# Kernel tuning notes

Hardware: AMD Instinct MI355X
Metric: run time of the kernel (lower is better)

## Reference

```python
import jax, jax.numpy as jnp
import numpy as np

B, D, F, P = 65536, 256, 512, 256


def setup_inputs() -> dict:
    key = jax.random.key(0)
    k_x, k_f, k_p, k_a, k_b, k_t = jax.random.split(key, 6)
    x = jax.random.normal(k_x, (B, D), dtype=jnp.float32)
    # reset_parameters: uniform(-0.27, 1)
    features = jax.random.uniform(k_f, (F, D), dtype=jnp.float32, minval=-0.27, maxval=1.0)
    prototypes = jax.random.uniform(k_p, (P, D), dtype=jnp.float32, minval=-0.27, maxval=1.0)
    # alpha/beta/theta init to zeros in the module; use small random values so the
    # output is non-trivial for kernel correctness checking.
    alpha = jax.random.normal(k_a, (1,), dtype=jnp.float32) * 0.1
    beta = jax.random.normal(k_b, (1,), dtype=jnp.float32) * 0.1
    theta = jax.random.normal(k_t, (1,), dtype=jnp.float32) * 0.1
    return {"x": x, "features": features, "prototypes": prototypes,
            "alpha": alpha, "beta": beta, "theta": theta}


def reference(x, features, prototypes, alpha, beta, theta):
    # Shared projections
    x_features = x @ features.T                 # [B, F]
    p_features = prototypes @ features.T        # [P, F]
    x_present = jax.nn.relu(x_features)         # [B, F]
    p_present = jax.nn.relu(p_features)         # [P, F]
    x_weighted = x_features * x_present         # [B, F]
    p_weighted = p_features * p_present         # [P, F]

    # Tversky terms
    common = x_weighted @ p_weighted.T                          # [B, P]
    x_weighted_sum = jnp.sum(x_weighted, axis=1, keepdims=True)  # [B, 1]
    x_p_interaction = x_weighted @ p_present.T                  # [B, P]
    x_distinctive = x_weighted_sum - x_p_interaction            # [B, P]
    p_weighted_sum = jnp.sum(p_weighted, axis=1)[None, :]        # [1, P]
    x_p_weighted_interaction = x_present @ p_weighted.T         # [B, P]
    p_distinctive = p_weighted_sum - x_p_weighted_interaction   # [B, P]

    return theta * common - alpha * x_distinctive - beta * p_distinctive
```

## Files before the change

### kernel.cpp

```cpp
#include <hip/hip_runtime.h>
#include <cstdint>
#include <cstddef>

#define Bsz 65536
#define Dsz 256
#define Fsz 512
#define Psz 256

typedef __attribute__((ext_vector_type(8))) short short8;
typedef __attribute__((ext_vector_type(4))) short short4v;
typedef __attribute__((ext_vector_type(4))) float float4v;
typedef __attribute__((ext_vector_type(16))) float float16v;
typedef __attribute__((ext_vector_type(4))) unsigned uint4v;

__device__ inline short f2bf(float f) {
    unsigned u = __builtin_bit_cast(unsigned, f);
    u = (u + 0x7FFFu + ((u >> 16) & 1u)) >> 16;
    return (short)u;
}
__device__ inline float bf2f(short s) {
    unsigned u = ((unsigned)(unsigned short)s) << 16;
    return __builtin_bit_cast(float, u);
}
__device__ inline unsigned cvt_pk_bf16(float lo, float hi) {
    unsigned r;
    asm("v_cvt_pk_bf16_f32 %0, %1, %2" : "=v"(r) : "v"(lo), "v"(hi));
    return r;
}
__device__ inline void gl_lds16(const short* g, short* lds) {
    __builtin_amdgcn_global_load_lds((const __attribute__((address_space(1))) unsigned*)g,
                                     (__attribute__((address_space(3))) unsigned*)lds,
                                     16, 0, 0);
}


#define SBPITCH 136

__global__ __launch_bounds__(256, 2) void k_pre(
    const float* __restrict__ prototypes, const float* __restrict__ features,
    const float* __restrict__ alpha_p, const float* __restrict__ beta_p,
    const float* __restrict__ theta_p,
    short* __restrict__ featbB, short* __restrict__ pab, float* __restrict__ pws_part)
{
    __shared__ char lds[65536 + 17408];
    short* FB = (short*)lds;
    short* As = (short*)(lds + 65536);
    short* Sb = (short*)(lds + 65536);

    const int t = threadIdx.x;
    const int w = t >> 6, lane = t & 63, l15 = lane & 15, l4 = lane >> 4;
    const int rowg = blockIdx.x >> 2, nc = blockIdx.x & 3;
    const float alpha = *alpha_p, beta = *beta_p, theta = *theta_p;

    #pragma unroll
    for (int it = 0; it < 16; ++it) {
        int u = it * 256 + t;
        int ftl = u >> 10, dtl = (u >> 6) & 15, ln = u & 63;
        const float* src = features + (size_t)(nc * 128 + ftl * 32 + (ln & 31)) * Dsz
                         + dtl * 16 + (ln >> 5) * 8;
        float4v v0 = *(const float4v*)src;
        float4v v1 = *(const float4v*)(src + 4);
        uint4v uv;
        uv.x = cvt_pk_bf16(v0.x, v0.y);
        uv.y = cvt_pk_bf16(v0.z, v0.w);
        uv.z = cvt_pk_bf16(v1.x, v1.y);
        uv.w = cvt_pk_bf16(v1.z, v1.w);
        short8 sv = __builtin_bit_cast(short8, uv);
        *(short8*)&FB[u * 8] = sv;
        if (rowg == 0) {
            int go = (((nc * 4 + ftl) * 16 + dtl) * 64 + ln) * 8;
            *(short8*)&featbB[go] = sv;
        }
    }

    float4v acc[2][4];
    #pragma unroll
    for (int a = 0; a < 2; ++a)
        #pragma unroll
        for (int b = 0; b < 4; ++b) acc[a][b] = (float4v){0.f, 0.f, 0.f, 0.f};

    const float* pbase = prototypes + (size_t)rowg * 64 * Dsz;

    for (int kc = 0; kc < 4; ++kc) {
        __syncthreads();
        #pragma unroll
        for (int j = 0; j < 4; ++j) {
            int idx = j * 1024 + t * 4;
            int r = idx >> 6, c = idx & 63;
            float4v v = *(const float4v*)(pbase + (size_t)r * Dsz + kc * 64 + c);
            int unit = r * 8 + ((c >> 3) ^ (r & 7));
            short4v s4; s4.x = f2bf(v.x); s4.y = f2bf(v.y); s4.z = f2bf(v.z); s4.w = f2bf(v.w);
            *(short4v*)((char*)As + unit * 16 + (c & 7) * 2) = s4;
        }
        __syncthreads();
        #pragma unroll
        for (int kk = 0; kk < 2; ++kk) {
            short8 af[2], bfr[4];
            const int k8 = kk * 4 + l4;
            #pragma unroll
            for (int tm = 0; tm < 2; ++tm) {
                int m = (w & 1) * 32 + tm * 16 + l15;
                af[tm] = *(const short8*)&As[(m * 8 + (k8 ^ (m & 7))) * 8];
            }
            #pragma unroll
            for (int tn = 0; tn < 4; ++tn) {
                int fl = ((w >> 1) * 4 + tn) * 16 + l15;
                int dtl = kc * 4 + kk * 2 + (l4 >> 1);
                int lnp = (fl & 31) + 32 * (l4 & 1);
                bfr[tn] = *(const short8*)&FB[(((fl >> 5) * 16 + dtl) * 64 + lnp) * 8];
            }
            #pragma unroll
            for (int tm = 0; tm < 2; ++tm)
                #pragma unroll
                for (int tn = 0; tn < 4; ++tn)
                    acc[tm][tn] = __builtin_amdgcn_mfma_f32_16x16x32_bf16(af[tm], bfr[tn], acc[tm][tn], 0, 0, 0);
        }
    }
    __syncthreads();
    #pragma unroll
    for (int tm = 0; tm < 2; ++tm)
        #pragma unroll
        for (int tn = 0; tn < 4; ++tn)
            #pragma unroll
            for (int r = 0; r < 4; ++r) {
                int row = (w & 1) * 32 + tm * 16 + l4 * 4 + r;
                int col = (w >> 1) * 64 + tn * 16 + l15;
                Sb[row * SBPITCH + col] = f2bf(acc[tm][tn][r]);
            }
    __syncthreads();
    #pragma unroll
    for (int rep = 0; rep < 4; ++rep) {
        int u = rep * 256 + t;
        int row = u >> 4, i = u & 15;
        short8 sv = *(const short8*)&Sb[row * SBPITCH + i * 8];
        uint4v u0, u1;
        float sum = 0.f;
        #pragma unroll
        for (int e = 0; e < 8; ++e) {
            float pf = bf2f(sv[e]);
            float pp = fmaxf(pf, 0.f);
            float pw = pf * pp;
            float a0 = theta * pw + alpha * (pp - 1.f);
            float b0 = beta * pw;
            sum += pw;
            unsigned pk = cvt_pk_bf16(a0, b0);
            if (e < 4) u0[e] = pk; else u1[e - 4] = pk;
        }
        int p = rowg * 64 + row;
        int c = 4 * nc + (i >> 2), s2 = i & 3, pt = p >> 5;
        int base = ((c * 4 + s2) * 8 + pt) * 512;
        *(short8*)&pab[base + (p & 31) * 8] = __builtin_bit_cast(short8, u0);
        *(short8*)&pab[base + ((p & 31) + 32) * 8] = __builtin_bit_cast(short8, u1);
        #pragma unroll
        for (int mk = 1; mk < 16; mk <<= 1) sum += __shfl_xor(sum, mk, 64);
        if (l15 == 0) pws_part[nc * 256 + p] = -beta * sum;
    }
}

__global__ __launch_bounds__(256, 2) void k_main(
    const float* __restrict__ x, const short* __restrict__ featbB,
    const short* __restrict__ pab, const float* __restrict__ pws_part,
    float* __restrict__ out)
{
    __shared__ short XL[16384];
    __shared__ short FBL[16384];

    const int t = threadIdx.x;
    const int w = t >> 6, lane = t & 63, l31 = lane & 31, h = lane >> 5;
    const size_t row0 = (size_t)blockIdx.x * 64;

    #pragma unroll
    for (int it = 0; it < 8; ++it) {
        int idx = it * 256 + t;
        int mt_i = idx >> 10, dt_i = (idx >> 6) & 15, ln = idx & 63;
        const float* src = x + (row0 + mt_i * 32 + (ln & 31)) * Dsz + dt_i * 16 + (ln >> 5) * 8;
        float4v v0 = *(const float4v*)src;
        float4v v1 = *(const float4v*)(src + 4);
        uint4v uv;
        uv.x = cvt_pk_bf16(v0.x, v0.y);
        uv.y = cvt_pk_bf16(v0.z, v0.w);
        uv.z = cvt_pk_bf16(v1.x, v1.y);
        uv.w = cvt_pk_bf16(v1.z, v1.w);
        *(short8*)&XL[idx * 8] = __builtin_bit_cast(short8, uv);
    }

    #pragma unroll
    for (int i = 0; i < 4; ++i) {
        int dt = w * 4 + i;
        gl_lds16(featbB + dt * 512 + lane * 8, &FBL[dt * 512]);
    }
    __syncthreads();

    const int mt = w & 1, pth = w >> 1;
    int xbase = mt * 8192 + lane * 8;
    const int lane8 = lane * 8;
    const int pboff = (pth * 4) * 512 + lane8;

    short8 xlo[8];
    #pragma unroll
    for (int dt = 0; dt < 8; ++dt)
        xlo[dt] = *(const short8*)&XL[xbase + dt * 512];

    float16v acc[4];
    #pragma unroll
    for (int a = 0; a < 4; ++a)
        #pragma unroll
        for (int e = 0; e < 16; ++e) acc[a][e] = 0.f;

    short8 PB[16];
    #pragma unroll
    for (int ptl = 0; ptl < 4; ++ptl)
        #pragma unroll
        for (int s = 0; s < 4; ++s)
            PB[ptl * 4 + s] = *(const short8*)(pab + pboff + s * 4096 + ptl * 512);

    #pragma unroll 1
    for (int c = 0; c < 16; ++c) {
        const int buf = (c & 1) * 8192;
        const int cn = (c + 1) & 15;

        if (c) __syncthreads();
        asm volatile("" : "+v"(xbase));

        {
            const short* gsrc = featbB + (size_t)cn * 8192 + lane8;
            short* ldst = &FBL[buf ^ 8192];
            #pragma unroll
            for (int i = 0; i < 4; ++i) {
                int dt = w * 4 + i;
                gl_lds16(gsrc + dt * 512, ldst + dt * 512);
            }
        }

        float16v C1;
        #pragma unroll
        for (int e = 0; e < 16; ++e) C1[e] = 0.f;
        #pragma unroll
        for (int g = 0; g < 4; ++g) {
            short8 fbf[4];
            #pragma unroll
            for (int i = 0; i < 4; ++i)
                fbf[i] = *(const short8*)&FBL[buf + (g * 4 + i) * 512 + lane8];
            __builtin_amdgcn_s_setprio(1);
            #pragma unroll
            for (int i = 0; i < 4; ++i) {
                const int dt = g * 4 + i;
                short8 xf = (dt < 8) ? xlo[dt] : *(const short8*)&XL[xbase + dt * 512];
                C1 = __builtin_amdgcn_mfma_f32_32x32x16_bf16(fbf[i], xf, C1, 0, 0, 0);
            }
            __builtin_amdgcn_s_setprio(0);
        }

        #pragma unroll
        for (int s = 0; s < 4; ++s) {
            uint4v uf;
            #pragma unroll
            for (int q = 0; q < 4; ++q) {
                float xf = C1[4 * s + q];
                float xp = fmaxf(xf, 0.f);
                uf[q] = cvt_pk_bf16(xf * xp, xp);
            }
            short8 A2f = __builtin_bit_cast(short8, uf);
            __builtin_amdgcn_s_setprio(1);
            #pragma unroll
            for (int ptl = 0; ptl < 4; ++ptl)
                acc[ptl] = __builtin_amdgcn_mfma_f32_32x32x16_bf16(A2f, PB[ptl * 4 + s], acc[ptl], 0, 0, 0);
            __builtin_amdgcn_s_setprio(0);
        }

        {
            const short* pbn = pab + (size_t)cn * 16384 + pboff;
            #pragma unroll
            for (int ptl = 0; ptl < 4; ++ptl)
                #pragma unroll
                for (int s = 0; s < 4; ++s)
                    PB[ptl * 4 + s] = *(const short8*)(pbn + s * 4096 + ptl * 512);
        }
    }

    #pragma unroll
    for (int ptl = 0; ptl < 4; ++ptl) {
        int pcol = (pth * 4 + ptl) * 32 + l31;
        float pn = pws_part[pcol] + pws_part[256 + pcol] + pws_part[512 + pcol] + pws_part[768 + pcol];
        #pragma unroll
        for (int r = 0; r < 16; ++r) {
            size_t m = row0 + mt * 32 + (r & 3) + 8 * (r >> 2) + 4 * h;
            out[m * Psz + pcol] = acc[ptl][r] + pn;
        }
    }
}

extern "C" void kernel_launch(void* const* d_in, const int* in_sizes, int n_in,
                              void* d_out, int out_size, void* d_ws, size_t ws_size,
                              hipStream_t stream) {
    const float* x          = (const float*)d_in[0];
    const float* features   = (const float*)d_in[1];
    const float* prototypes = (const float*)d_in[2];
    const float* alpha      = (const float*)d_in[3];
    const float* beta       = (const float*)d_in[4];
    const float* theta      = (const float*)d_in[5];
    float* out = (float*)d_out;

    char* ws = (char*)d_ws;
    short* featbB   = (short*)(ws);
    short* pab      = (short*)(ws + 262144);
    float* pws_part = (float*)(ws + 786432);

    hipLaunchKernelGGL(k_pre,  dim3(16),   dim3(256), 0, stream,
                       prototypes, features, alpha, beta, theta, featbB, pab, pws_part);
    hipLaunchKernelGGL(k_main, dim3(1024), dim3(256), 0, stream,
                       x, featbB, pab, pws_part, out);
}
```

Measured before the change: 192.7 us.

## Enlarge block to 128 rows, keep x in registers, stage prototypes in LDS

Each block now covers 128 rows with 512 threads (8 waves, 4 row tiles by 2 prototype halves). Each wave loads its x rows directly into registers as bf16 fragments instead of going through LDS. The precomputed prototype operand is double-buffered in LDS alongside the features chunk, replacing per-wave global register loads. The first GEMM is split across two accumulators to break the MFMA dependency chain. The goal is to halve feature/prototype traffic per row and cut global-load latency, at the cost of more LDS and register pressure, which may limit occupancy.

```diff
diff --git a/kernel.cpp b/kernel.cpp
--- a/kernel.cpp
+++ b/kernel.cpp
@@ -157,130 +157,126 @@
     }
 }
 
-__global__ __launch_bounds__(256, 2) void k_main(
+__global__ __launch_bounds__(512, 2) void k_main(
     const float* __restrict__ x, const short* __restrict__ featbB,
     const short* __restrict__ pab, const float* __restrict__ pws_part,
     float* __restrict__ out)
 {
-    __shared__ short XL[16384];
-    __shared__ short FBL[16384];
+    __shared__ short FBL[2][8192];
+    __shared__ short PBL[2][16384];
 
     const int t = threadIdx.x;
     const int w = t >> 6, lane = t & 63, l31 = lane & 31, h = lane >> 5;
-    const size_t row0 = (size_t)blockIdx.x * 64;
-
-    #pragma unroll
-    for (int it = 0; it < 8; ++it) {
-        int idx = it * 256 + t;
-        int mt_i = idx >> 10, dt_i = (idx >> 6) & 15, ln = idx & 63;
-        const float* src = x + (row0 + mt_i * 32 + (ln & 31)) * Dsz + dt_i * 16 + (ln >> 5) * 8;
-        float4v v0 = *(const float4v*)src;
-        float4v v1 = *(const float4v*)(src + 4);
-        uint4v uv;
-        uv.x = cvt_pk_bf16(v0.x, v0.y);
-        uv.y = cvt_pk_bf16(v0.z, v0.w);
-        uv.z = cvt_pk_bf16(v1.x, v1.y);
-        uv.w = cvt_pk_bf16(v1.z, v1.w);
-        *(short8*)&XL[idx * 8] = __builtin_bit_cast(short8, uv);
-    }
-
-    #pragma unroll
-    for (int i = 0; i < 4; ++i) {
-        int dt = w * 4 + i;
-        gl_lds16(featbB + dt * 512 + lane * 8, &FBL[dt * 512]);
-    }
-    __syncthreads();
-
-    const int mt = w & 1, pth = w >> 1;
-    int xbase = mt * 8192 + lane * 8;
+    const int mt = w & 3, pth4 = (w >> 2) * 4;
+    const size_t row0 = (size_t)blockIdx.x * 128;
     const int lane8 = lane * 8;
-    const int pboff = (pth * 4) * 512 + lane8;
-
-    short8 xlo[8];
-    #pragma unroll
-    for (int dt = 0; dt < 8; ++dt)
-        xlo[dt] = *(const short8*)&XL[xbase + dt * 512];
+
+    {
+        const short* fsrc = featbB + lane8;
+        gl_lds16(fsrc + (2 * w) * 512,     &FBL[0][(2 * w) * 512]);
+        gl_lds16(fsrc + (2 * w + 1) * 512, &FBL[0][(2 * w + 1) * 512]);
+        const short* psrc = pab + lane8;
+        #pragma unroll
+        for (int i = 0; i < 4; ++i)
+            gl_lds16(psrc + (4 * w + i) * 512, &PBL[0][(4 * w + i) * 512]);
+    }
+    __builtin_amdgcn_sched_barrier(0);
+
+    short8 xf[16];
+    {
+        const float* xr = x + (row0 + mt * 32 + l31) * Dsz + h * 8;
+        #pragma unroll
+        for (int dt = 0; dt < 16; ++dt) {
+            float4v v0 = *(const float4v*)(xr + dt * 16);
+            float4v v1 = *(const float4v*)(xr + dt * 16 + 4);
+            uint4v uv;
+            uv.x = cvt_pk_bf16(v0.x, v0.y);
+            uv.y = cvt_pk_bf16(v0.z, v0.w);
+            uv.z = cvt_pk_bf16(v1.x, v1.y);
+            uv.w = cvt_pk_bf16(v1.z, v1.w);
+            xf[dt] = __builtin_bit_cast(short8, uv);
+        }
+    }
 
     float16v acc[4];
     #pragma unroll
     for (int a = 0; a < 4; ++a)
         #pragma unroll
         for (int e = 0; e < 16; ++e) acc[a][e] = 0.f;
-
-    short8 PB[16];
-    #pragma unroll
-    for (int ptl = 0; ptl < 4; ++ptl)
-        #pragma unroll
-        for (int s = 0; s < 4; ++s)
-            PB[ptl * 4 + s] = *(const short8*)(pab + pboff + s * 4096 + ptl * 512);
 
     #pragma unroll 1
     for (int c = 0; c < 16; ++c) {
-        const int buf = (c & 1) * 8192;
+        const int cur = c & 1, nxt = cur ^ 1;
         const int cn = (c + 1) & 15;
 
-        if (c) __syncthreads();
-        asm volatile("" : "+v"(xbase));
+        __syncthreads();
 
         {
-            const short* gsrc = featbB + (size_t)cn * 8192 + lane8;
-            short* ldst = &FBL[buf ^ 8192];
-            #pragma unroll
-            for (int i = 0; i < 4; ++i) {
-                int dt = w * 4 + i;
-                gl_lds16(gsrc + dt * 512, ldst + dt * 512);
-            }
-        }
-
-        float16v C1;
-        #pragma unroll
-        for (int e = 0; e < 16; ++e) C1[e] = 0.f;
+            const short* fsrc = featbB + cn * 8192 + lane8;
+            gl_lds16(fsrc + (2 * w) * 512,     &FBL[nxt][(2 * w) * 512]);
+            gl_lds16(fsrc + (2 * w + 1) * 512, &FBL[nxt][(2 * w + 1) * 512]);
+            const short* psrc = pab + (size_t)cn * 16384 + lane8;
+            #pragma unroll
+            for (int i = 0; i < 4; ++i)
+                gl_lds16(psrc + (4 * w + i) * 512, &PBL[nxt][(4 * w + i) * 512]);
+        }
+        __builtin_amdgcn_sched_barrier(0);
+
+        float16v C1a, C1b;
+        #pragma unroll
+        for (int e = 0; e < 16; ++e) { C1a[e] = 0.f; C1b[e] = 0.f; }
+        short8 PBr[8];
         #pragma unroll
         for (int g = 0; g < 4; ++g) {
             short8 fbf[4];
             #pragma unroll
             for (int i = 0; i < 4; ++i)
-                fbf[i] = *(const short8*)&FBL[buf + (g * 4 + i) * 512 + lane8];
+                fbf[i] = *(const short8*)&FBL[cur][(g * 4 + i) * 512 + lane8];
+            if (g == 2) {
+                #pragma unroll
+                for (int k = 0; k < 8; ++k)
+                    PBr[k] = *(const short8*)&PBL[cur][(((k >> 2)) * 8 + pth4 + (k & 3)) * 512 + lane8];
+            }
             __builtin_amdgcn_s_setprio(1);
             #pragma unroll
             for (int i = 0; i < 4; ++i) {
-                const int dt = g * 4 + i;
-                short8 xf = (dt < 8) ? xlo[dt] : *(const short8*)&XL[xbase + dt * 512];
-                C1 = __builtin_amdgcn_mfma_f32_32x32x16_bf16(fbf[i], xf, C1, 0, 0, 0);
+                if (((g * 4 + i) & 1) == 0)
+                    C1a = __builtin_amdgcn_mfma_f32_32x32x16_bf16(fbf[i], xf[g * 4 + i], C1a, 0, 0, 0);
+                else
+                    C1b = __builtin_amdgcn_mfma_f32_32x32x16_bf16(fbf[i], xf[g * 4 + i], C1b, 0, 0, 0);
             }
             __builtin_amdgcn_s_setprio(0);
         }
+        float16v C1;
+        #pragma unroll
+        for (int e = 0; e < 16; ++e) C1[e] = C1a[e] + C1b[e];
 
         #pragma unroll
         for (int s = 0; s < 4; ++s) {
+            if (s == 2) {
+                #pragma unroll
+                for (int k = 0; k < 8; ++k)
+                    PBr[k] = *(const short8*)&PBL[cur][((2 + (k >> 2)) * 8 + pth4 + (k & 3)) * 512 + lane8];
+            }
             uint4v uf;
             #pragma unroll
             for (int q = 0; q < 4; ++q) {
-                float xf = C1[4 * s + q];
-                float xp = fmaxf(xf, 0.f);
-                uf[q] = cvt_pk_bf16(xf * xp, xp);
+                float xv = C1[4 * s + q];
+                float xp = fmaxf(xv, 0.f);
+                uf[q] = cvt_pk_bf16(xv * xp, xp);
             }
             short8 A2f = __builtin_bit_cast(short8, uf);
             __builtin_amdgcn_s_setprio(1);
             #pragma unroll
             for (int ptl = 0; ptl < 4; ++ptl)
-                acc[ptl] = __builtin_amdgcn_mfma_f32_32x32x16_bf16(A2f, PB[ptl * 4 + s], acc[ptl], 0, 0, 0);
+                acc[ptl] = __builtin_amdgcn_mfma_f32_32x32x16_bf16(A2f, PBr[(s & 1) * 4 + ptl], acc[ptl], 0, 0, 0);
             __builtin_amdgcn_s_setprio(0);
         }
-
-        {
-            const short* pbn = pab + (size_t)cn * 16384 + pboff;
-            #pragma unroll
-            for (int ptl = 0; ptl < 4; ++ptl)
-                #pragma unroll
-                for (int s = 0; s < 4; ++s)
-                    PB[ptl * 4 + s] = *(const short8*)(pbn + s * 4096 + ptl * 512);
-        }
     }
 
     #pragma unroll
     for (int ptl = 0; ptl < 4; ++ptl) {
-        int pcol = (pth * 4 + ptl) * 32 + l31;
+        int pcol = (pth4 + ptl) * 32 + l31;
         float pn = pws_part[pcol] + pws_part[256 + pcol] + pws_part[512 + pcol] + pws_part[768 + pcol];
         #pragma unroll
         for (int r = 0; r < 16; ++r) {
@@ -306,8 +302,8 @@
     short* pab      = (short*)(ws + 262144);
     float* pws_part = (float*)(ws + 786432);
 
-    hipLaunchKernelGGL(k_pre,  dim3(16),   dim3(256), 0, stream,
+    hipLaunchKernelGGL(k_pre,  dim3(16),  dim3(256), 0, stream,
                        prototypes, features, alpha, beta, theta, featbB, pab, pws_part);
-    hipLaunchKernelGGL(k_main, dim3(1024), dim3(256), 0, stream,
+    hipLaunchKernelGGL(k_main, dim3(512), dim3(512), 0, stream,
                        x, featbB, pab, pws_part, out);
 }
```

New measurement: 198.4 us. 3.0% more time.
